# Optimization experiments

Hardware: AMD Instinct MI355X
Metric: run time of the kernel (lower is better)

## Reference

```python
import jax, jax.numpy as jnp
import numpy as np

NUM_HEADS = 8
WS = 7          # window size (hardcoded in source)
SR = 4          # sr_ratio
EPS = 1e-5


def _win_partition(t, ws, H, W):
    # t: [B, h, N, d] -> [B*h*nW, ws*ws, d]
    B, h, N, d = t.shape
    t = t.reshape(B * h, H // ws, ws, W // ws, ws, d)
    t = t.transpose(0, 1, 3, 2, 4, 5)
    return t.reshape(-1, ws * ws, d)


def _win_reverse(w, ws, H, W, h):
    # w: [B*h*nW, ws*ws, d] -> [B, H*W, h*d]
    d = w.shape[-1]
    Bh = w.shape[0] // ((H // ws) * (W // ws))
    x = w.reshape(Bh, H // ws, W // ws, ws, ws, d).transpose(0, 1, 3, 2, 4, 5)
    x = x.reshape(Bh // h, h, H, W, d).transpose(0, 2, 3, 1, 4)
    return x.reshape(Bh // h, H * W, h * d)


def setup_inputs() -> dict:
    key = jax.random.key(0)
    B, H, W, C = 32, 56, 56, 256
    N = H * W
    ks = jax.random.split(key, 10)
    s = lambda k, shp: jax.random.normal(k, shp, dtype=jnp.float32) * 0.02
    return {
        "x": jax.random.normal(ks[0], (B, N, C), dtype=jnp.float32),
        "lepe_lin_w": s(ks[1], (C, C)), "lepe_lin_b": jnp.zeros((C,), jnp.float32),
        "lepe_conv_w": s(ks[2], (3, 3, 1, C)), "lepe_conv_b": jnp.zeros((C,), jnp.float32),
        "sr_w": s(ks[3], (SR, SR, C, C)), "sr_b": jnp.zeros((C,), jnp.float32),
        "norm_g": jnp.ones((C,), jnp.float32), "norm_b": jnp.zeros((C,), jnp.float32),
        "q1_w": s(ks[4], (C, C // 2)), "kv1_w": s(ks[5], (C, C)),
        "q2_w": s(ks[6], (C, C // 2)), "kv2_w": s(ks[7], (C, C)),
        "proj_w": s(ks[8], (C, C)), "proj_b": jnp.zeros((C,), jnp.float32),
        "H": H, "W": W,
    }


def reference(x, lepe_lin_w, lepe_lin_b, lepe_conv_w, lepe_conv_b, sr_w, sr_b,
              norm_g, norm_b, q1_w, kv1_w, q2_w, kv2_w, proj_w, proj_b, H, W):
    B, N, C = x.shape
    h2 = NUM_HEADS // 2
    d = C // NUM_HEADS
    scale = d ** (-0.5)

    # lepe: linear -> depthwise 3x3 conv (NHWC) -> flatten back
    lep = (x @ lepe_lin_w + lepe_lin_b).reshape(B, H, W, C)
    lep = jax.lax.conv_general_dilated(
        lep, lepe_conv_w, window_strides=(1, 1), padding='SAME',
        dimension_numbers=('NHWC', 'HWIO', 'NHWC'), feature_group_count=C) + lepe_conv_b
    lepe = lep.reshape(B, N, C)

    # --- branch 1: global attention over sr-downsampled kv ---
    q1 = (x @ q1_w).reshape(B, N, h2, d).transpose(0, 2, 1, 3)         # [B,h2,N,d]
    img = x.reshape(B, H, W, C)
    x1_ = jax.lax.conv_general_dilated(
        img, sr_w, window_strides=(SR, SR), padding='VALID',
        dimension_numbers=('NHWC', 'HWIO', 'NHWC')) + sr_b              # [B,H/sr,W/sr,C]
    x1_ = x1_.reshape(B, -1, C)                                         # [B,N1,C]
    mu = jnp.mean(x1_, axis=-1, keepdims=True)
    var = jnp.mean(jnp.square(x1_ - mu), axis=-1, keepdims=True)
    x1_ = (x1_ - mu) * jax.lax.rsqrt(var + EPS) * norm_g + norm_b
    x1_ = jax.nn.gelu(x1_, approximate=False)
    kv1 = (x1_ @ kv1_w).reshape(B, -1, 2, h2, d).transpose(2, 0, 3, 1, 4)
    k1, v1 = kv1[0], kv1[1]                                             # [B,h2,N1,d]
    attn1 = jax.nn.softmax(jnp.einsum('bhnd,bhmd->bhnm', q1, k1) * scale, axis=-1)
    x1 = jnp.einsum('bhnm,bhmd->bhnd', attn1, v1)
    x1 = x1.transpose(0, 2, 1, 3).reshape(B, N, C // 2)

    # --- branch 2: 7x7 window attention ---
    q2 = (x @ q2_w).reshape(B, N, h2, d).transpose(0, 2, 1, 3)          # [B,h2,N,d]
    kv2 = (x @ kv2_w).reshape(B, -1, 2, h2, d).transpose(2, 0, 3, 1, 4)
    k2, v2 = kv2[0], kv2[1]
    q2w = _win_partition(q2, WS, H, W)                                  # [B*h2*nW,49,d]
    k2w = _win_partition(k2, WS, H, W)
    v2w = _win_partition(v2, WS, H, W)
    attn2 = jax.nn.softmax(jnp.einsum('wnd,wmd->wnm', q2w, k2w) * scale, axis=-1)
    x2w = jnp.einsum('wnm,wmd->wnd', attn2, v2w)
    x2 = _win_reverse(x2w, WS, H, W, h2)                                # [B,N,C/2]

    out = jnp.concatenate([x1, x2], axis=-1)
    out = (out + lepe) @ proj_w + proj_b
    return out
```

## Files before the change

kernel.cpp:

```cpp
#include <hip/hip_runtime.h>
#include <hip/hip_bf16.h>

typedef __hip_bfloat16 bf16;
typedef __attribute__((ext_vector_type(8))) short short8;
typedef __attribute__((ext_vector_type(4))) float floatx4;

__device__ __forceinline__ float toF(bf16 v){ return __bfloat162float(v); }
__device__ __forceinline__ float b2f(unsigned short u){
  return __uint_as_float(((unsigned int)u) << 16);
}
__device__ __forceinline__ unsigned short f2bu(float f){
  bf16 h = __float2bfloat16(f);
  return *(unsigned short*)&h;
}
__device__ __forceinline__ void storeT(bf16* p, float v){ *p = __float2bfloat16(v); }
__device__ __forceinline__ void storeT(float* p, float v){ *p = v; }

__global__ __launch_bounds__(256) void cvt_x_kernel(
    const float* __restrict__ in, bf16* __restrict__ out) {
  size_t i4 = ((size_t)blockIdx.x * 256 + threadIdx.x) * 4;
  float4 v = *(const float4*)(in + i4);
  ushort4 o;
  o.x = f2bu(v.x); o.y = f2bu(v.y); o.z = f2bu(v.z); o.w = f2bu(v.w);
  *(ushort4*)(out + i4) = o;
}

__global__ __launch_bounds__(256) void cvt_tr_kernel(
    const float* __restrict__ src, bf16* __restrict__ dst, int K, int N) {
  int idx = blockIdx.x * 256 + threadIdx.x;
  int k = idx / N, n = idx - k * N;
  dst[(size_t)n * K + k] = __float2bfloat16(src[idx]);
}

__global__ __launch_bounds__(256) void srbase_kernel(int* __restrict__ base) {
  int t = blockIdx.x * 256 + threadIdx.x;
  if (t >= 6272) return;
  int b = t / 196, p = t - b * 196;
  int oy = p / 14, ox = p - oy * 14;
  base[t] = ((b * 56 + oy * 4) * 56 + ox * 4) * 256;
}

template<typename OT>
__global__ __launch_bounds__(256) void gemm_mfma(
    const bf16* __restrict__ A, const bf16* __restrict__ BT,
    const float* __restrict__ bias, OT* __restrict__ C,
    int M, int K, int N) {
  __shared__ uint4 As[128 * 5];
  __shared__ uint4 Bs[128 * 5];
  const int tid = threadIdx.x;
  const int m0 = blockIdx.y * 128;
  const int n0 = blockIdx.x * 128;
  const int wave = tid >> 6, lane = tid & 63;
  const int wm = (wave >> 1) * 64, wn = (wave & 1) * 64;
  const int l15 = lane & 15, quad = lane >> 4;
  floatx4 zero = {0.f, 0.f, 0.f, 0.f};
  floatx4 acc[4][4];
#pragma unroll
  for (int i = 0; i < 4; i++)
#pragma unroll
    for (int j = 0; j < 4; j++) acc[i][j] = zero;

  for (int k0 = 0; k0 < K; k0 += 32) {
#pragma unroll
    for (int it = 0; it < 2; it++) {
      int id = it * 256 + tid;
      int row = id >> 2, seg = id & 3;
      As[row * 5 + seg] = *(const uint4*)(A + (size_t)(m0 + row) * K + k0 + seg * 8);
      Bs[row * 5 + seg] = *(const uint4*)(BT + (size_t)(n0 + row) * K + k0 + seg * 8);
    }
    __syncthreads();
    short8 af[4], bfr[4];
#pragma unroll
    for (int i = 0; i < 4; i++)
      af[i] = *(const short8*)&As[(wm + i * 16 + l15) * 5 + quad];
#pragma unroll
    for (int j = 0; j < 4; j++)
      bfr[j] = *(const short8*)&Bs[(wn + j * 16 + l15) * 5 + quad];
#pragma unroll
    for (int i = 0; i < 4; i++)
#pragma unroll
      for (int j = 0; j < 4; j++)
        acc[i][j] = __builtin_amdgcn_mfma_f32_16x16x32_bf16(af[i], bfr[j], acc[i][j], 0, 0, 0);
    __syncthreads();
  }
#pragma unroll
  for (int j = 0; j < 4; j++) {
    int n = n0 + wn + j * 16 + l15;
    float bv = bias ? bias[n] : 0.0f;
#pragma unroll
    for (int i = 0; i < 4; i++) {
      int m = m0 + wm + i * 16 + quad * 4;
#pragma unroll
      for (int r = 0; r < 4; r++)
        storeT(&C[(size_t)(m + r) * N + n], acc[i][j][r] + bv);
    }
  }
}

__global__ __launch_bounds__(256) void gemm_sr(
    const bf16* __restrict__ X, const bf16* __restrict__ BT,
    const int* __restrict__ base, float* __restrict__ C) {
  __shared__ uint4 As[128 * 5];
  __shared__ uint4 Bs[128 * 5];
  __shared__ int sBase[128];
  const int tid = threadIdx.x;
  const int m0 = blockIdx.y * 128;
  const int n0 = blockIdx.x * 128;
  const int kz = blockIdx.z;
  if (tid < 128) sBase[tid] = base[m0 + tid];
  const int wave = tid >> 6, lane = tid & 63;
  const int wm = (wave >> 1) * 64, wn = (wave & 1) * 64;
  const int l15 = lane & 15, quad = lane >> 4;
  floatx4 zero = {0.f, 0.f, 0.f, 0.f};
  floatx4 acc[4][4];
#pragma unroll
  for (int i = 0; i < 4; i++)
#pragma unroll
    for (int j = 0; j < 4; j++) acc[i][j] = zero;
  __syncthreads();

  const int kbeg = kz * 512;
  for (int k0 = kbeg; k0 < kbeg + 512; k0 += 32) {
#pragma unroll
    for (int it = 0; it < 2; it++) {
      int id = it * 256 + tid;
      int row = id >> 2, seg = id & 3;
      int k = k0 + seg * 8;
      int kp = k >> 8, c = k & 255;
      int off = ((kp >> 2) * 56 + (kp & 3)) * 256 + c;
      As[row * 5 + seg] = *(const uint4*)(X + (size_t)sBase[row] + off);
      Bs[row * 5 + seg] = *(const uint4*)(BT + (size_t)(n0 + row) * 4096 + k);
    }
    __syncthreads();
    short8 af[4], bfr[4];
#pragma unroll
    for (int i = 0; i < 4; i++)
      af[i] = *(const short8*)&As[(wm + i * 16 + l15) * 5 + quad];
#pragma unroll
    for (int j = 0; j < 4; j++)
      bfr[j] = *(const short8*)&Bs[(wn + j * 16 + l15) * 5 + quad];
#pragma unroll
    for (int i = 0; i < 4; i++)
#pragma unroll
      for (int j = 0; j < 4; j++)
        acc[i][j] = __builtin_amdgcn_mfma_f32_16x16x32_bf16(af[i], bfr[j], acc[i][j], 0, 0, 0);
    __syncthreads();
  }
  float* Cp = C + (size_t)kz * (6272 * 256);
#pragma unroll
  for (int j = 0; j < 4; j++) {
    int n = n0 + wn + j * 16 + l15;
#pragma unroll
    for (int i = 0; i < 4; i++) {
      int m = m0 + wm + i * 16 + quad * 4;
#pragma unroll
      for (int r = 0; r < 4; r++)
        Cp[(size_t)(m + r) * 256 + n] = acc[i][j][r];
    }
  }
}

__global__ __launch_bounds__(256) void gemm_proj_mfma(
    const bf16* __restrict__ X1, const bf16* __restrict__ X2,
    const bf16* __restrict__ L2, const bf16* __restrict__ BT,
    const float* __restrict__ bias, float* __restrict__ C) {
  __shared__ uint4 As[128 * 5];
  __shared__ uint4 Bs[128 * 5];
  const int tid = threadIdx.x;
  const int m0 = blockIdx.y * 128;
  const int n0 = blockIdx.x * 128;
  const int wave = tid >> 6, lane = tid & 63;
  const int wm = (wave >> 1) * 64, wn = (wave & 1) * 64;
  const int l15 = lane & 15, quad = lane >> 4;
  floatx4 zero = {0.f, 0.f, 0.f, 0.f};
  floatx4 acc[4][4];
#pragma unroll
  for (int i = 0; i < 4; i++)
#pragma unroll
    for (int j = 0; j < 4; j++) acc[i][j] = zero;

  for (int k0 = 0; k0 < 256; k0 += 32) {
#pragma unroll
    for (int it = 0; it < 2; it++) {
      int id = it * 256 + tid;
      int row = id >> 2, seg = id & 3;
      int k = k0 + seg * 8;
      int mrow = m0 + row;
      const bf16* src = (k < 128) ? X1 + (size_t)mrow * 128 + k
                                  : X2 + (size_t)mrow * 128 + (k - 128);
      uint4 va = *(const uint4*)src;
      uint4 vl = *(const uint4*)(L2 + (size_t)mrow * 256 + k);
      const unsigned short* pa = (const unsigned short*)&va;
      const unsigned short* pl = (const unsigned short*)&vl;
      unsigned short ov[8];
#pragma unroll
      for (int e = 0; e < 8; e++) ov[e] = f2bu(b2f(pa[e]) + b2f(pl[e]));
      As[row * 5 + seg] = *(const uint4*)ov;
      Bs[row * 5 + seg] = *(const uint4*)(BT + (size_t)(n0 + row) * 256 + k);
    }
    __syncthreads();
    short8 af[4], bfr[4];
#pragma unroll
    for (int i = 0; i < 4; i++)
      af[i] = *(const short8*)&As[(wm + i * 16 + l15) * 5 + quad];
#pragma unroll
    for (int j = 0; j < 4; j++)
      bfr[j] = *(const short8*)&Bs[(wn + j * 16 + l15) * 5 + quad];
#pragma unroll
    for (int i = 0; i < 4; i++)
#pragma unroll
      for (int j = 0; j < 4; j++)
        acc[i][j] = __builtin_amdgcn_mfma_f32_16x16x32_bf16(af[i], bfr[j], acc[i][j], 0, 0, 0);
    __syncthreads();
  }
#pragma unroll
  for (int j = 0; j < 4; j++) {
    int n = n0 + wn + j * 16 + l15;
    float bv = bias[n];
#pragma unroll
    for (int i = 0; i < 4; i++) {
      int m = m0 + wm + i * 16 + quad * 4;
#pragma unroll
      for (int r = 0; r < 4; r++)
        C[(size_t)(m + r) * 256 + n] = acc[i][j][r] + bv;
    }
  }
}

__global__ __launch_bounds__(256) void dwconv8_kernel(
    const bf16* __restrict__ in, const float* __restrict__ w,
    const float* __restrict__ bias, bf16* __restrict__ out) {
  const int idx = blockIdx.x * 256 + threadIdx.x;
  const int c8 = (idx & 31) * 8;
  const int sp = idx >> 5;
  const int xx = sp % 56;
  const int yb = sp / 56;
  const int yy = yb % 56;
  const int b  = yb / 56;
  float4 bb0 = *(const float4*)&bias[c8];
  float4 bb1 = *(const float4*)&bias[c8 + 4];
  float acc[8] = {bb0.x, bb0.y, bb0.z, bb0.w, bb1.x, bb1.y, bb1.z, bb1.w};
#pragma unroll
  for (int dy = 0; dy < 3; dy++) {
    int y = yy + dy - 1;
    if ((unsigned)y >= 56u) continue;
#pragma unroll
    for (int dx = 0; dx < 3; dx++) {
      int x = xx + dx - 1;
      if ((unsigned)x >= 56u) continue;
      uint4 v = *(const uint4*)&in[((size_t)((b * 56 + y) * 56 + x)) * 256 + c8];
      const unsigned short* pv = (const unsigned short*)&v;
      float4 w0 = *(const float4*)&w[(dy * 3 + dx) * 256 + c8];
      float4 w1 = *(const float4*)&w[(dy * 3 + dx) * 256 + c8 + 4];
      float wf[8] = {w0.x, w0.y, w0.z, w0.w, w1.x, w1.y, w1.z, w1.w};
#pragma unroll
      for (int e = 0; e < 8; e++) acc[e] += b2f(pv[e]) * wf[e];
    }
  }
  unsigned short o[8];
#pragma unroll
  for (int e = 0; e < 8; e++) o[e] = f2bu(acc[e]);
  *(uint4*)&out[(size_t)sp * 256 + c8] = *(const uint4*)o;
}

__global__ __launch_bounds__(256) void ln_gelu_kernel(
    const float* __restrict__ in, const float* __restrict__ srb,
    const float* __restrict__ g, const float* __restrict__ bb,
    bf16* __restrict__ out) {
  const int tok = blockIdx.x;
  const int tid = threadIdx.x;
  float v = srb[tid];
  const float* p = in + (size_t)tok * 256 + tid;
#pragma unroll
  for (int c = 0; c < 8; c++) v += p[(size_t)c * 1605632];
  float s = v, s2 = v * v;
#pragma unroll
  for (int o = 32; o > 0; o >>= 1) {
    s += __shfl_down(s, o, 64);
    s2 += __shfl_down(s2, o, 64);
  }
  __shared__ float rs[4], rs2[4];
  int wid = tid >> 6, lane = tid & 63;
  if (lane == 0) { rs[wid] = s; rs2[wid] = s2; }
  __syncthreads();
  float tot = rs[0] + rs[1] + rs[2] + rs[3];
  float tot2 = rs2[0] + rs2[1] + rs2[2] + rs2[3];
  float mean = tot * (1.0f / 256.0f);
  float var = tot2 * (1.0f / 256.0f) - mean * mean;
  float y = (v - mean) * rsqrtf(var + 1e-5f) * g[tid] + bb[tid];
  out[(size_t)tok * 256 + tid] =
      __float2bfloat16(0.5f * y * (1.0f + erff(y * 0.70710678118654752f)));
}

__global__ __launch_bounds__(256) void attn1_mfma(
    const bf16* __restrict__ Q12, const float* __restrict__ KV,
    bf16* __restrict__ O) {
  __shared__ bf16 sk[224 * 32];
  __shared__ bf16 svT[32 * 232];
  __shared__ bf16 pbuf[4][64 * 32];
  const int b = blockIdx.z, h = blockIdx.y, chunk = blockIdx.x;
  const int tid = threadIdx.x;
  const int wave = tid >> 6, lane = tid & 63;
  const int l15 = lane & 15, quad = lane >> 4;
  for (int i = tid; i < 224 * 8; i += 256) {
    int m = i >> 3, c = i & 7;
    float4 kf = {0.f, 0.f, 0.f, 0.f}, vf = {0.f, 0.f, 0.f, 0.f};
    if (m < 196) {
      const float* p = KV + ((size_t)(b * 196 + m)) * 256 + h * 32 + c * 4;
      kf = *(const float4*)p;
      vf = *(const float4*)(p + 128);
    }
    ushort4 ko;
    ko.x = f2bu(kf.x); ko.y = f2bu(kf.y); ko.z = f2bu(kf.z); ko.w = f2bu(kf.w);
    *(ushort4*)&sk[m * 32 + c * 4] = ko;
    svT[(c * 4 + 0) * 232 + m] = __float2bfloat16(vf.x);
    svT[(c * 4 + 1) * 232 + m] = __float2bfloat16(vf.y);
    svT[(c * 4 + 2) * 232 + m] = __float2bfloat16(vf.z);
    svT[(c * 4 + 3) * 232 + m] = __float2bfloat16(vf.w);
  }
  __syncthreads();
  const int q0 = chunk * 256 + wave * 64;
  short8 aq[4];
#pragma unroll
  for (int i = 0; i < 4; i++) {
    int qr = q0 + i * 16 + l15; if (qr > 3135) qr = 3135;
    aq[i] = *(const short8*)(Q12 + ((size_t)(b * 3136 + qr)) * 256 + h * 32 + quad * 8);
  }
  const float scale = 0.17677669529663687f;
  floatx4 zero = {0.f, 0.f, 0.f, 0.f};
  floatx4 acc[4][2];
  float lsum[4][4];
#pragma unroll
  for (int i = 0; i < 4; i++) {
    acc[i][0] = zero; acc[i][1] = zero;
#pragma unroll
    for (int r = 0; r < 4; r++) lsum[i][r] = 0.f;
  }
  bf16* pw = pbuf[wave];
  for (int c = 0; c < 7; c++) {
    const int kv0 = c * 32;
    short8 bk[2];
#pragma unroll
    for (int n = 0; n < 2; n++)
      bk[n] = *(const short8*)&sk[(kv0 + n * 16 + l15) * 32 + quad * 8];
    floatx4 s[4][2];
#pragma unroll
    for (int i = 0; i < 4; i++)
#pragma unroll
      for (int n = 0; n < 2; n++)
        s[i][n] = __builtin_amdgcn_mfma_f32_16x16x32_bf16(aq[i], bk[n], zero, 0, 0, 0);
#pragma unroll
    for (int i = 0; i < 4; i++)
#pragma unroll
      for (int n = 0; n < 2; n++) {
        bool valid = (kv0 + n * 16 + l15) < 196;
#pragma unroll
        for (int r = 0; r < 4; r++) {
          float p = valid ? __expf(s[i][n][r] * scale) : 0.f;
          lsum[i][r] += p;
          pw[(i * 16 + quad * 4 + r) * 32 + n * 16 + l15] = __float2bfloat16(p);
        }
      }
    asm volatile("s_waitcnt lgkmcnt(0)" ::: "memory");
    short8 ap[4], bv[2];
#pragma unroll
    for (int i = 0; i < 4; i++)
      ap[i] = *(const short8*)&pw[(i * 16 + l15) * 32 + quad * 8];
#pragma unroll
    for (int n = 0; n < 2; n++)
      bv[n] = *(const short8*)&svT[(n * 16 + l15) * 232 + kv0 + quad * 8];
#pragma unroll
    for (int i = 0; i < 4; i++)
#pragma unroll
      for (int n = 0; n < 2; n++)
        acc[i][n] = __builtin_amdgcn_mfma_f32_16x16x32_bf16(ap[i], bv[n], acc[i][n], 0, 0, 0);
  }
#pragma unroll
  for (int i = 0; i < 4; i++)
#pragma unroll
    for (int r = 0; r < 4; r++) {
      float v = lsum[i][r];
      v += __shfl_xor(v, 1, 64);
      v += __shfl_xor(v, 2, 64);
      v += __shfl_xor(v, 4, 64);
      v += __shfl_xor(v, 8, 64);
      lsum[i][r] = 1.0f / v;
    }
#pragma unroll
  for (int i = 0; i < 4; i++)
#pragma unroll
    for (int r = 0; r < 4; r++) {
      int qr = q0 + i * 16 + quad * 4 + r;
      if (qr < 3136) {
        bf16* op = O + ((size_t)(b * 3136 + qr)) * 128 + h * 32;
        op[l15]      = __float2bfloat16(acc[i][0][r] * lsum[i][r]);
        op[16 + l15] = __float2bfloat16(acc[i][1][r] * lsum[i][r]);
      }
    }
}

__global__ __launch_bounds__(256) void attn2_mfma(
    const bf16* __restrict__ Q12, const bf16* __restrict__ KV2,
    bf16* __restrict__ O) {
  __shared__ bf16 sk[64 * 136];
  __shared__ bf16 pb[4][64 * 72];
  const int b = blockIdx.y;
  const int win = blockIdx.x;
  const int wy = win >> 3, wx = win & 7;
  const int tid = threadIdx.x;
  const int wave = tid >> 6, lane = tid & 63;
  const int l15 = lane & 15, quad = lane >> 4;
  const int h = wave;

  for (int i = tid; i < 49 * 16; i += 256) {
    int m = i >> 4, c = i & 15;
    int iy = m / 7, ix = m - iy * 7;
    int n = (wy * 7 + iy) * 56 + wx * 7 + ix;
    *(uint4*)&sk[m * 136 + c * 8] =
        *(const uint4*)&KV2[((size_t)(b * 3136 + n)) * 256 + c * 8];
  }

  short8 bvv[2][2];
#pragma unroll
  for (int ks = 0; ks < 2; ks++)
#pragma unroll
    for (int nt = 0; nt < 2; nt++)
#pragma unroll
      for (int e = 0; e < 8; e++) {
        int k = ks * 32 + quad * 8 + e; if (k > 48) k = 48;
        int iy = k / 7, ix = k - iy * 7;
        int n = (wy * 7 + iy) * 56 + wx * 7 + ix;
        bvv[ks][nt][e] = ((const short*)KV2)[((size_t)(b * 3136 + n)) * 256
                                             + 128 + h * 32 + nt * 16 + l15];
      }

  short8 aq[4];
#pragma unroll
  for (int i = 0; i < 4; i++) {
    int lq = i * 16 + l15; if (lq > 48) lq = 48;
    int iy = lq / 7, ix = lq - iy * 7;
    int n = (wy * 7 + iy) * 56 + wx * 7 + ix;
    aq[i] = *(const short8*)(Q12 + ((size_t)(b * 3136 + n)) * 256 + 128 + h * 32 + quad * 8);
  }
  __syncthreads();

  const float scale = 0.17677669529663687f;
  floatx4 zero = {0.f, 0.f, 0.f, 0.f};
  floatx4 acc[4][2];
  float lsum[4][4];
#pragma unroll
  for (int i = 0; i < 4; i++) {
    acc[i][0] = zero; acc[i][1] = zero;
#pragma unroll
    for (int r = 0; r < 4; r++) lsum[i][r] = 0.f;
  }
  bf16* pw = pb[wave];
#pragma unroll
  for (int c = 0; c < 2; c++) {
    const int kv0 = c * 32;
    short8 bk[2];
#pragma unroll
    for (int n = 0; n < 2; n++)
      bk[n] = *(const short8*)&sk[(kv0 + n * 16 + l15) * 136 + h * 32 + quad * 8];
    floatx4 s[4][2];
#pragma unroll
    for (int i = 0; i < 4; i++)
#pragma unroll
      for (int n = 0; n < 2; n++)
        s[i][n] = __builtin_amdgcn_mfma_f32_16x16x32_bf16(aq[i], bk[n], zero, 0, 0, 0);
#pragma unroll
    for (int i = 0; i < 4; i++)
#pragma unroll
      for (int n = 0; n < 2; n++) {
        bool valid = (kv0 + n * 16 + l15) < 49;
#pragma unroll
        for (int r = 0; r < 4; r++) {
          float p = valid ? __expf(s[i][n][r] * scale) : 0.f;
          lsum[i][r] += p;
          pw[(i * 16 + quad * 4 + r) * 72 + kv0 + n * 16 + l15] = __float2bfloat16(p);
        }
      }
  }
  asm volatile("s_waitcnt lgkmcnt(0)" ::: "memory");
#pragma unroll
  for (int ks = 0; ks < 2; ks++) {
    short8 ap[4];
#pragma unroll
    for (int i = 0; i < 4; i++)
      ap[i] = *(const short8*)&pw[(i * 16 + l15) * 72 + ks * 32 + quad * 8];
#pragma unroll
    for (int i = 0; i < 4; i++)
#pragma unroll
      for (int nt = 0; nt < 2; nt++)
        acc[i][nt] = __builtin_amdgcn_mfma_f32_16x16x32_bf16(ap[i], bvv[ks][nt], acc[i][nt], 0, 0, 0);
  }
#pragma unroll
  for (int i = 0; i < 4; i++)
#pragma unroll
    for (int r = 0; r < 4; r++) {
      float v = lsum[i][r];
      v += __shfl_xor(v, 1, 64);
      v += __shfl_xor(v, 2, 64);
      v += __shfl_xor(v, 4, 64);
      v += __shfl_xor(v, 8, 64);
      lsum[i][r] = 1.0f / v;
    }
#pragma unroll
  for (int i = 0; i < 4; i++)
#pragma unroll
    for (int r = 0; r < 4; r++) {
      int lq = i * 16 + quad * 4 + r;
      if (lq < 49) {
        int iy = lq / 7, ix = lq - iy * 7;
        int n = (wy * 7 + iy) * 56 + wx * 7 + ix;
        bf16* op = O + ((size_t)(b * 3136 + n)) * 128 + h * 32;
        op[l15]      = __float2bfloat16(acc[i][0][r] * lsum[i][r]);
        op[16 + l15] = __float2bfloat16(acc[i][1][r] * lsum[i][r]);
      }
    }
}

extern "C" void kernel_launch(void* const* d_in, const int* in_sizes, int n_in,
                              void* d_out, int out_size, void* d_ws, size_t ws_size,
                              hipStream_t stream) {
  const float* x           = (const float*)d_in[0];
  const float* lepe_lin_w  = (const float*)d_in[1];
  const float* lepe_lin_b  = (const float*)d_in[2];
  const float* lepe_conv_w = (const float*)d_in[3];
  const float* lepe_conv_b = (const float*)d_in[4];
  const float* sr_w        = (const float*)d_in[5];
  const float* sr_b        = (const float*)d_in[6];
  const float* norm_g      = (const float*)d_in[7];
  const float* norm_b      = (const float*)d_in[8];
  const float* q1_w        = (const float*)d_in[9];
  const float* kv1_w       = (const float*)d_in[10];
  const float* q2_w        = (const float*)d_in[11];
  const float* kv2_w       = (const float*)d_in[12];
  const float* proj_w      = (const float*)d_in[13];
  const float* proj_b      = (const float*)d_in[14];
  float* out = (float*)d_out;

  char* ws = (char*)d_ws;
  char* ob = (char*)d_out;
  const size_t szBNC = 100352ull * 256 * 2;
  const size_t szBNh = 100352ull * 128 * 2;
  bf16*  xb  = (bf16*)ob;
  bf16*  Q12 = (bf16*)(ob + szBNC);
  bf16*  L1  = (bf16*)ws;
  bf16*  KV2 = (bf16*)ws;
  float* X1Ppart = (float*)ws;
  bf16*  X1N = (bf16*)ob;
  float* KV1 = (float*)(ob + 8388608);
  bf16*  X1  = (bf16*)ws;
  bf16*  L2  = (bf16*)(ws + szBNC);
  bf16*  X2  = (bf16*)(ws + 2 * szBNC);
  char*  wtb = ws + 2 * szBNC + szBNh;
  bf16* wT_lepe = (bf16*)(wtb);
  bf16* wT_q12  = (bf16*)(wtb + 131072);
  bf16* wT_kv1  = (bf16*)(wtb + 262144);
  bf16* wT_kv2  = (bf16*)(wtb + 393216);
  bf16* wT_proj = (bf16*)(wtb + 524288);
  bf16* wT_sr   = (bf16*)(wtb + 655360);
  int*  srbase  = (int*)(wtb + 655360 + 2097152);

  cvt_x_kernel<<<25088, 256, 0, stream>>>(x, xb);
  cvt_tr_kernel<<<256, 256, 0, stream>>>(lepe_lin_w, wT_lepe, 256, 256);
  cvt_tr_kernel<<<128, 256, 0, stream>>>(q1_w, wT_q12, 256, 128);
  cvt_tr_kernel<<<128, 256, 0, stream>>>(q2_w, wT_q12 + 128 * 256, 256, 128);
  cvt_tr_kernel<<<256, 256, 0, stream>>>(kv1_w, wT_kv1, 256, 256);
  cvt_tr_kernel<<<256, 256, 0, stream>>>(kv2_w, wT_kv2, 256, 256);
  cvt_tr_kernel<<<256, 256, 0, stream>>>(proj_w, wT_proj, 256, 256);
  cvt_tr_kernel<<<4096, 256, 0, stream>>>(sr_w, wT_sr, 4096, 256);
  srbase_kernel<<<25, 256, 0, stream>>>(srbase);

  gemm_mfma<bf16><<<dim3(2, 784), 256, 0, stream>>>(
      xb, wT_lepe, lepe_lin_b, L1, 100352, 256, 256);
  dwconv8_kernel<<<12544, 256, 0, stream>>>(L1, lepe_conv_w, lepe_conv_b, L2);

  gemm_mfma<bf16><<<dim3(2, 784), 256, 0, stream>>>(
      xb, wT_kv2, nullptr, KV2, 100352, 256, 256);
  gemm_mfma<bf16><<<dim3(2, 784), 256, 0, stream>>>(
      xb, wT_q12, nullptr, Q12, 100352, 256, 256);

  attn2_mfma<<<dim3(64, 32), 256, 0, stream>>>(Q12, KV2, X2);

  gemm_sr<<<dim3(2, 49, 8), 256, 0, stream>>>(xb, wT_sr, srbase, X1Ppart);
  ln_gelu_kernel<<<6272, 256, 0, stream>>>(X1Ppart, sr_b, norm_g, norm_b, X1N);
  gemm_mfma<float><<<dim3(2, 49), 256, 0, stream>>>(
      X1N, wT_kv1, nullptr, KV1, 6272, 256, 256);
  attn1_mfma<<<dim3(13, 4, 32), 256, 0, stream>>>(Q12, KV1, X1);

  gemm_proj_mfma<<<dim3(2, 784), 256, 0, stream>>>(
      X1, X2, L2, wT_proj, proj_b, out);
}
```

Baseline: 561.2 us.

## Fuse lepe, kv2 and q12 projections into one GEMM with swizzled block order

Concatenates the lepe, kv2 and q1/q2 weight matrices into one 768-wide transposed weight and runs a single GEMM over x, routing each 256-column segment to its own output buffer. A 1D grid with an XCD-aware swizzle is used so that blocks sharing the same A rows are scheduled close together, and the proj GEMM gets the same swizzle. This removes two kernel launches and lets A tiles be reused across output segments via cache. KV2 moves into a separate workspace region because L1 and KV2 are now live at the same time.

New measurement: 547.9 us. -2.4%, faster.

```diff
diff --git a/kernel.cpp b/kernel.cpp
--- a/kernel.cpp
+++ b/kernel.cpp
@@ -93,6 +93,67 @@
 #pragma unroll
       for (int r = 0; r < 4; r++)
         storeT(&C[(size_t)(m + r) * N + n], acc[i][j][r] + bv);
+    }
+  }
+}
+
+__global__ __launch_bounds__(256) void gemm_x3(
+    const bf16* __restrict__ A, const bf16* __restrict__ BT,
+    const float* __restrict__ lepe_b,
+    bf16* __restrict__ L1, bf16* __restrict__ KV2, bf16* __restrict__ Q12) {
+  __shared__ uint4 As[128 * 5];
+  __shared__ uint4 Bs[128 * 5];
+  const int sw = (blockIdx.x & 7) * 588 + (blockIdx.x >> 3);
+  const int bx = sw % 6, by = sw / 6;
+  const int m0 = by * 128;
+  const int n0 = bx * 128;
+  const int tid = threadIdx.x;
+  const int wave = tid >> 6, lane = tid & 63;
+  const int wm = (wave >> 1) * 64, wn = (wave & 1) * 64;
+  const int l15 = lane & 15, quad = lane >> 4;
+  floatx4 zero = {0.f, 0.f, 0.f, 0.f};
+  floatx4 acc[4][4];
+#pragma unroll
+  for (int i = 0; i < 4; i++)
+#pragma unroll
+    for (int j = 0; j < 4; j++) acc[i][j] = zero;
+
+  for (int k0 = 0; k0 < 256; k0 += 32) {
+#pragma unroll
+    for (int it = 0; it < 2; it++) {
+      int id = it * 256 + tid;
+      int row = id >> 2, seg = id & 3;
+      As[row * 5 + seg] = *(const uint4*)(A + (size_t)(m0 + row) * 256 + k0 + seg * 8);
+      Bs[row * 5 + seg] = *(const uint4*)(BT + (size_t)(n0 + row) * 256 + k0 + seg * 8);
+    }
+    __syncthreads();
+    short8 af[4], bfr[4];
+#pragma unroll
+    for (int i = 0; i < 4; i++)
+      af[i] = *(const short8*)&As[(wm + i * 16 + l15) * 5 + quad];
+#pragma unroll
+    for (int j = 0; j < 4; j++)
+      bfr[j] = *(const short8*)&Bs[(wn + j * 16 + l15) * 5 + quad];
+#pragma unroll
+    for (int i = 0; i < 4; i++)
+#pragma unroll
+      for (int j = 0; j < 4; j++)
+        acc[i][j] = __builtin_amdgcn_mfma_f32_16x16x32_bf16(af[i], bfr[j], acc[i][j], 0, 0, 0);
+    __syncthreads();
+  }
+  const int segN = n0 >> 8;
+  bf16* Cd = (segN == 0) ? L1 : (segN == 1) ? KV2 : Q12;
+  const int nc0 = n0 & 255;
+#pragma unroll
+  for (int j = 0; j < 4; j++) {
+    int nl = nc0 + wn + j * 16 + l15;
+    float bv = (segN == 0) ? lepe_b[nl] : 0.0f;
+#pragma unroll
+    for (int i = 0; i < 4; i++) {
+      int m = m0 + wm + i * 16 + quad * 4;
+#pragma unroll
+      for (int r = 0; r < 4; r++)
+        Cd[(size_t)(m + r) * 256 + nl] = __float2bfloat16(acc[i][j][r] + bv);
     }
   }
 }
@@ -166,9 +227,10 @@
     const float* __restrict__ bias, float* __restrict__ C) {
   __shared__ uint4 As[128 * 5];
   __shared__ uint4 Bs[128 * 5];
+  const int sw = (blockIdx.x & 7) * 196 + (blockIdx.x >> 3);
   const int tid = threadIdx.x;
-  const int m0 = blockIdx.y * 128;
-  const int n0 = blockIdx.x * 128;
+  const int m0 = (sw >> 1) * 128;
+  const int n0 = (sw & 1) * 128;
   const int wave = tid >> 6, lane = tid & 63;
   const int wm = (wave >> 1) * 64, wn = (wave & 1) * 64;
   const int l15 = lane & 15, quad = lane >> 4;
@@ -547,7 +609,6 @@
   bf16*  xb  = (bf16*)ob;
   bf16*  Q12 = (bf16*)(ob + szBNC);
   bf16*  L1  = (bf16*)ws;
-  bf16*  KV2 = (bf16*)ws;
   float* X1Ppart = (float*)ws;
   bf16*  X1N = (bf16*)ob;
   float* KV1 = (float*)(ob + 8388608);
@@ -555,32 +616,26 @@
   bf16*  L2  = (bf16*)(ws + szBNC);
   bf16*  X2  = (bf16*)(ws + 2 * szBNC);
   char*  wtb = ws + 2 * szBNC + szBNh;
-  bf16* wT_lepe = (bf16*)(wtb);
-  bf16* wT_q12  = (bf16*)(wtb + 131072);
-  bf16* wT_kv1  = (bf16*)(wtb + 262144);
-  bf16* wT_kv2  = (bf16*)(wtb + 393216);
+  bf16* wT_x    = (bf16*)(wtb);
+  bf16* wT_kv1  = (bf16*)(wtb + 393216);
   bf16* wT_proj = (bf16*)(wtb + 524288);
   bf16* wT_sr   = (bf16*)(wtb + 655360);
   int*  srbase  = (int*)(wtb + 655360 + 2097152);
+  bf16* KV2     = (bf16*)(wtb + 655360 + 2097152 + 32768);
 
   cvt_x_kernel<<<25088, 256, 0, stream>>>(x, xb);
-  cvt_tr_kernel<<<256, 256, 0, stream>>>(lepe_lin_w, wT_lepe, 256, 256);
-  cvt_tr_kernel<<<128, 256, 0, stream>>>(q1_w, wT_q12, 256, 128);
-  cvt_tr_kernel<<<128, 256, 0, stream>>>(q2_w, wT_q12 + 128 * 256, 256, 128);
+  cvt_tr_kernel<<<256, 256, 0, stream>>>(lepe_lin_w, wT_x, 256, 256);
+  cvt_tr_kernel<<<256, 256, 0, stream>>>(kv2_w, wT_x + 256 * 256, 256, 256);
+  cvt_tr_kernel<<<128, 256, 0, stream>>>(q1_w, wT_x + 512 * 256, 256, 128);
+  cvt_tr_kernel<<<128, 256, 0, stream>>>(q2_w, wT_x + 640 * 256, 256, 128);
   cvt_tr_kernel<<<256, 256, 0, stream>>>(kv1_w, wT_kv1, 256, 256);
-  cvt_tr_kernel<<<256, 256, 0, stream>>>(kv2_w, wT_kv2, 256, 256);
   cvt_tr_kernel<<<256, 256, 0, stream>>>(proj_w, wT_proj, 256, 256);
   cvt_tr_kernel<<<4096, 256, 0, stream>>>(sr_w, wT_sr, 4096, 256);
   srbase_kernel<<<25, 256, 0, stream>>>(srbase);
 
-  gemm_mfma<bf16><<<dim3(2, 784), 256, 0, stream>>>(
-      xb, wT_lepe, lepe_lin_b, L1, 100352, 256, 256);
+  gemm_x3<<<4704, 256, 0, stream>>>(xb, wT_x, lepe_lin_b, L1, KV2, Q12);
+
   dwconv8_kernel<<<12544, 256, 0, stream>>>(L1, lepe_conv_w, lepe_conv_b, L2);
-
-  gemm_mfma<bf16><<<dim3(2, 784), 256, 0, stream>>>(
-      xb, wT_kv2, nullptr, KV2, 100352, 256, 256);
-  gemm_mfma<bf16><<<dim3(2, 784), 256, 0, stream>>>(
-      xb, wT_q12, nullptr, Q12, 100352, 256, 256);
 
   attn2_mfma<<<dim3(64, 32), 256, 0, stream>>>(Q12, KV2, X2);
 
@@ -590,6 +645,6 @@
       X1N, wT_kv1, nullptr, KV1, 6272, 256, 256);
   attn1_mfma<<<dim3(13, 4, 32), 256, 0, stream>>>(Q12, KV1, X1);
 
-  gemm_proj_mfma<<<dim3(2, 784), 256, 0, stream>>>(
+  gemm_proj_mfma<<<1568, 256, 0, stream>>>(
       X1, X2, L2, wT_proj, proj_b, out);
 }
```
